# Performance work log

Hardware: AMD Instinct MI355X
Metric: run time of the kernel (lower is better)

Reference implementation:

```python
import jax, jax.numpy as jnp
import numpy as np

NODES_PER_GRAPH = 116
HEADS = 2
D_HEAD = 116  # out_channels per head
HID = 256
B = 512
N = B * NODES_PER_GRAPH
DEG = 8
E = N * DEG
D_OUT = HEADS * D_HEAD  # 232


def setup_inputs() -> dict:
    key = jax.random.key(0)
    ks = jax.random.split(key, 6)
    h_flat = jax.random.normal(ks[0], (N, HID), dtype=jnp.float32)
    # every node receives DEG edges from random nodes within its own 116-node graph
    dst = jnp.repeat(jnp.arange(N, dtype=jnp.int64), DEG)
    offs = jax.random.randint(ks[1], (E,), 0, NODES_PER_GRAPH, dtype=jnp.int64)
    src = (dst // NODES_PER_GRAPH) * NODES_PER_GRAPH + offs
    edge_index = jnp.stack([src, dst], axis=0)
    batch_index = jnp.repeat(jnp.arange(B, dtype=jnp.int64), NODES_PER_GRAPH)
    s = 1.0 / np.sqrt(HID)
    Wq = jax.random.normal(ks[2], (HID, D_OUT), dtype=jnp.float32) * s
    Wk = jax.random.normal(ks[3], (HID, D_OUT), dtype=jnp.float32) * s
    Wv = jax.random.normal(ks[4], (HID, D_OUT), dtype=jnp.float32) * s
    Ws = jax.random.normal(ks[5], (HID, D_OUT), dtype=jnp.float32) * s
    return {"h_flat": h_flat, "edge_index": edge_index, "batch_index": batch_index,
            "Wq": Wq, "Wk": Wk, "Wv": Wv, "Ws": Ws}


def _graph_transformer_layer(h, edge_index, Wq, Wk, Wv, Ws):
    # PyG TransformerConv-style multi-head edge attention, concat heads + root skip.
    n = h.shape[0]
    q = (h @ Wq).reshape(n, HEADS, D_HEAD)
    k = (h @ Wk).reshape(n, HEADS, D_HEAD)
    v = (h @ Wv).reshape(n, HEADS, D_HEAD)
    src, dst = edge_index[0], edge_index[1]
    # per-edge scores [E, H]
    scores = jnp.einsum('ehd,ehd->eh', q[dst], k[src]) / np.sqrt(D_HEAD)
    # segment softmax over incoming edges of each dst node
    m = jax.ops.segment_max(scores, dst, num_segments=n)
    m = jnp.where(jnp.isfinite(m), m, 0.0)
    ex = jnp.exp(scores - m[dst])
    denom = jax.ops.segment_sum(ex, dst, num_segments=n)
    alpha_e = ex / (denom[dst] + 1e-16)
    msg = alpha_e[:, :, None] * v[src]                      # [E, H, Dh]
    attn = jax.ops.segment_sum(msg, dst, num_segments=n)    # [N, H, Dh]
    return attn.reshape(n, D_OUT) + h @ Ws


def reference(h_flat, edge_index, batch_index, Wq, Wk, Wv, Ws):
    n = h_flat.shape[0]
    b = n // NODES_PER_GRAPH
    h_proj = _graph_transformer_layer(h_flat, edge_index, Wq, Wk, Wv, Ws)  # [N, 232]
    e = h_proj.mean(axis=-1)                                 # [N]
    # scatter_softmax over per-graph node segments
    em = jax.ops.segment_max(e, batch_index, num_segments=b)
    ee = jnp.exp(e - em[batch_index])
    es = jax.ops.segment_sum(ee, batch_index, num_segments=b)
    alpha = ee / es[batch_index]                             # [N]
    h_weighted = alpha[:, None] * h_proj                     # [N, 232]
    alpha_map = alpha.reshape(b, NODES_PER_GRAPH)            # [B, 116]
    return alpha_map, h_weighted
```

## Files before the change

### kernel.cpp

```cpp
#include <hip/hip_runtime.h>

#define NODES  116
#define HEADS  2
#define DH     116
#define HID    256
#define NGRAPH 512
#define NN     (NGRAPH*NODES)
#define DEG    8
#define DOUT   (HEADS*DH)
#define RSTR   136

typedef short  s8v  __attribute__((ext_vector_type(8)));
typedef float  f4v  __attribute__((ext_vector_type(4)));

static __device__ __forceinline__ float bf2f(unsigned short u) {
    union { unsigned int i; float f; } c; c.i = ((unsigned int)u) << 16; return c.f;
}
static __device__ __forceinline__ unsigned short f2bf(float f) {
    union { float f; unsigned int u; } c; c.f = f;
    unsigned int u = c.u;
    unsigned int r = (u + 0x7FFFu + ((u >> 16) & 1u)) >> 16;
    return (unsigned short)r;
}

#define GLD_LDS16(gptr, lptr) \
    __builtin_amdgcn_global_load_lds((const __attribute__((address_space(1))) void*)(gptr), \
                                     (__attribute__((address_space(3))) void*)(lptr), 16, 0, 0)

__global__ __launch_bounds__(256) void prep_w(const float* __restrict__ Wq,
                                              const float* __restrict__ Wk,
                                              const float* __restrict__ Wv,
                                              const float* __restrict__ Ws,
                                              unsigned short* __restrict__ wt)
{
    unsigned int f = blockIdx.x * 256 + threadIdx.x;
    unsigned int n    = f & 127;
    unsigned int quad = (f >> 7) & 3;
    unsigned int kb   = (f >> 9) & 7;
    unsigned int ch   = (f >> 12) & 3;
    unsigned int hd   = f >> 14;
    unsigned short o[8] = {0,0,0,0,0,0,0,0};
    if (n < NODES) {
        unsigned int col = hd * DH + n;
        unsigned int k   = kb * 32 + quad * 8;
        const float* W = (ch == 0) ? Wq : (ch == 1) ? Wk : (ch == 2) ? Wv : Ws;
        #pragma unroll
        for (int i = 0; i < 8; i++)
            o[i] = f2bf(W[(size_t)(k + i) * DOUT + col]);
    }
    *(uint4*)(wt + (size_t)f * 8) = *(const uint4*)o;
}

__global__ __launch_bounds__(1024, 4) void fused_all(
    const float* __restrict__ h,
    const unsigned short* __restrict__ wt,
    const int* __restrict__ eidx,
    unsigned short* __restrict__ hp,
    float* __restrict__ out_alpha,
    float* __restrict__ out_hw)
{
    __shared__ __align__(16) unsigned short stA[8*4096];
    __shared__ __align__(16) unsigned short ovl[2*128*RSTR];
    __shared__ int   srcl[NODES*DEG];
    __shared__ float scf[NODES*DEG];
    __shared__ float ps[2][NODES];
    __shared__ float red[2];

    unsigned short* const ql = ovl;
    unsigned short* const kl = ovl + 128 * RSTR;

    const int g   = blockIdx.x;
    const int tid = threadIdx.x;
    const int w    = tid >> 6;
    const int lane = tid & 63;
    const int l15  = lane & 15;
    const int quad = lane >> 4;
    const int wm   = w >> 2;
    const int wn   = w & 3;

    if (tid < NODES * DEG)
        srcl[tid] = eidx[(size_t)g * NODES * DEG + tid] - g * NODES;

    {
        const int am = tid >> 3;
        const int q8 = tid & 7;
        long grow = (long)g * NODES + am;
        if (grow >= NN) grow = NN - 1;
        const float* hrow = h + (size_t)grow * HID + q8 * 4;
        const int aoff = ((q8 >> 1) * 128 + am) * 8 + (q8 & 1) * 4;
        float4 a8[8];
        #pragma unroll
        for (int kb = 0; kb < 8; kb++) a8[kb] = *(const float4*)(hrow + kb * 32);
        #pragma unroll
        for (int kb = 0; kb < 8; kb++) {
            unsigned short o[4] = { f2bf(a8[kb].x), f2bf(a8[kb].y),
                                    f2bf(a8[kb].z), f2bf(a8[kb].w) };
            *(uint2*)(stA + kb * 4096 + aoff) = *(const uint2*)o;
        }
    }

    #pragma unroll
    for (int hd = 0; hd < 2; hd++) {
        const size_t wbase = (size_t)hd * 4 * 8 * 4096;

        f4v accq[2][2], acck[2][2], accv[2][2], accs[2][2];
        #pragma unroll
        for (int i = 0; i < 2; i++)
            #pragma unroll
            for (int j = 0; j < 2; j++)
                #pragma unroll
                for (int r = 0; r < 4; r++) {
                    accq[i][j][r] = 0.f; acck[i][j][r] = 0.f;
                    accv[i][j][r] = 0.f; accs[i][j][r] = 0.f;
                }

        #pragma unroll
        for (int j = 0; j < 2; j++) {
            int c = w * 2 + j;
            int ch = c >> 3, sub = c & 7;
            const unsigned short* src = wt + wbase + ((size_t)(ch * 8)) * 4096 + sub * 512;
            GLD_LDS16((const char*)src + lane * 16, (char*)ovl + c * 1024);
        }
        __syncthreads();

        #pragma unroll
        for (int kb = 0; kb < 8; kb++) {
            const unsigned short* curb = ovl + (kb & 1) * 16384;
            unsigned short* nxtb = ovl + ((kb & 1) ^ 1) * 16384;
            if (kb < 7) {
                #pragma unroll
                for (int j = 0; j < 2; j++) {
                    int c = w * 2 + j;
                    int ch = c >> 3, sub = c & 7;
                    const unsigned short* src = wt + wbase + ((size_t)(ch * 8 + kb + 1)) * 4096 + sub * 512;
                    GLD_LDS16((const char*)src + lane * 16, (char*)nxtb + c * 1024);
                }
            }
            const unsigned short* sa = stA + kb * 4096;
            s8v a0 = *(const s8v*)(sa + (quad * 128 + wm * 32 + l15) * 8);
            s8v a1 = *(const s8v*)(sa + (quad * 128 + wm * 32 + 16 + l15) * 8);
            #define CHUNK_MFMA(ACC, CH) { \
                s8v b0 = *(const s8v*)(curb + (CH) * 4096 + (quad * 128 + wn * 32 + l15) * 8); \
                s8v b1 = *(const s8v*)(curb + (CH) * 4096 + (quad * 128 + wn * 32 + 16 + l15) * 8); \
                ACC[0][0] = __builtin_amdgcn_mfma_f32_16x16x32_bf16(a0, b0, ACC[0][0], 0, 0, 0); \
                ACC[0][1] = __builtin_amdgcn_mfma_f32_16x16x32_bf16(a0, b1, ACC[0][1], 0, 0, 0); \
                ACC[1][0] = __builtin_amdgcn_mfma_f32_16x16x32_bf16(a1, b0, ACC[1][0], 0, 0, 0); \
                ACC[1][1] = __builtin_amdgcn_mfma_f32_16x16x32_bf16(a1, b1, ACC[1][1], 0, 0, 0); }
            CHUNK_MFMA(accq, 0)
            CHUNK_MFMA(acck, 1)
            CHUNK_MFMA(accv, 2)
            CHUNK_MFMA(accs, 3)
            #undef CHUNK_MFMA
            __syncthreads();
        }

        #pragma unroll
        for (int i = 0; i < 2; i++) {
            #pragma unroll
            for (int j = 0; j < 2; j++) {
                int col = wn * 32 + j * 16 + l15;
                #pragma unroll
                for (int r = 0; r < 4; r++) {
                    int row = wm * 32 + i * 16 + quad * 4 + r;
                    ql[row * RSTR + col] = (col < NODES) ? f2bf(accq[i][j][r]) : 0;
                    kl[row * RSTR + col] = (col < NODES) ? f2bf(acck[i][j][r]) : 0;
                }
            }
        }
        __syncthreads();

        f4v sacc[2][2];
        #pragma unroll
        for (int i = 0; i < 2; i++)
            #pragma unroll
            for (int j = 0; j < 2; j++)
                #pragma unroll
                for (int r = 0; r < 4; r++) sacc[i][j][r] = 0.f;
        #pragma unroll
        for (int ks = 0; ks < 4; ks++) {
            s8v a0 = *(const s8v*)(ql + (wm * 32 + l15) * RSTR + ks * 32 + quad * 8);
            s8v a1 = *(const s8v*)(ql + (wm * 32 + 16 + l15) * RSTR + ks * 32 + quad * 8);
            s8v b0 = *(const s8v*)(kl + (wn * 32 + l15) * RSTR + ks * 32 + quad * 8);
            s8v b1 = *(const s8v*)(kl + (wn * 32 + 16 + l15) * RSTR + ks * 32 + quad * 8);
            sacc[0][0] = __builtin_amdgcn_mfma_f32_16x16x32_bf16(a0, b0, sacc[0][0], 0, 0, 0);
            sacc[0][1] = __builtin_amdgcn_mfma_f32_16x16x32_bf16(a0, b1, sacc[0][1], 0, 0, 0);
            sacc[1][0] = __builtin_amdgcn_mfma_f32_16x16x32_bf16(a1, b0, sacc[1][0], 0, 0, 0);
            sacc[1][1] = __builtin_amdgcn_mfma_f32_16x16x32_bf16(a1, b1, sacc[1][1], 0, 0, 0);
        }
        #pragma unroll
        for (int i = 0; i < 2; i++) {
            #pragma unroll
            for (int r = 0; r < 4; r++) {
                int row = wm * 32 + i * 16 + quad * 4 + r;
                if (row < NODES) {
                    #pragma unroll
                    for (int j = 0; j < 2; j++) {
                        int col = wn * 32 + j * 16 + l15;
                        #pragma unroll
                        for (int e = 0; e < DEG; e++)
                            if (srcl[row * DEG + e] == col)
                                scf[row * DEG + e] = sacc[i][j][r];
                    }
                }
            }
        }
        __syncthreads();

        for (int f = tid; f < 128 * RSTR / 8; f += 1024)
            *(uint4*)(kl + (size_t)f * 8) = make_uint4(0u, 0u, 0u, 0u);
        #pragma unroll
        for (int i = 0; i < 2; i++) {
            #pragma unroll
            for (int j = 0; j < 2; j++) {
                int col = wn * 32 + j * 16 + l15;
                #pragma unroll
                for (int r = 0; r < 4; r++) {
                    int row = wm * 32 + i * 16 + quad * 4 + r;
                    ql[col * RSTR + row] = (row < NODES) ? f2bf(accv[i][j][r]) : 0;
                }
            }
        }
        __syncthreads();

        if (tid < NODES * DEG) {
            float s = scf[tid] * 0.09284766908852594f;
            float m = s;
            m = fmaxf(m, __shfl_xor(m, 1));
            m = fmaxf(m, __shfl_xor(m, 2));
            m = fmaxf(m, __shfl_xor(m, 4));
            float e = __expf(s - m);
            float sum = e;
            sum += __shfl_xor(sum, 1);
            sum += __shfl_xor(sum, 2);
            sum += __shfl_xor(sum, 4);
            scf[tid] = e / sum;
        }
        __syncthreads();

        if (tid < NODES) {
            #pragma unroll
            for (int j = 0; j < DEG; j++) {
                int sj = srcl[tid * DEG + j];
                bool first = true;
                for (int jj = 0; jj < j; jj++) first = first && (srcl[tid * DEG + jj] != sj);
                if (first) {
                    float a = scf[tid * DEG + j];
                    for (int jj = j + 1; jj < DEG; jj++)
                        if (srcl[tid * DEG + jj] == sj) a += scf[tid * DEG + jj];
                    kl[tid * RSTR + sj] = f2bf(a);
                }
            }
        }
        __syncthreads();

        #pragma unroll
        for (int ks = 0; ks < 4; ks++) {
            s8v a0 = *(const s8v*)(kl + (wm * 32 + l15) * RSTR + ks * 32 + quad * 8);
            s8v a1 = *(const s8v*)(kl + (wm * 32 + 16 + l15) * RSTR + ks * 32 + quad * 8);
            s8v b0 = *(const s8v*)(ql + (wn * 32 + l15) * RSTR + ks * 32 + quad * 8);
            s8v b1 = *(const s8v*)(ql + (wn * 32 + 16 + l15) * RSTR + ks * 32 + quad * 8);
            accs[0][0] = __builtin_amdgcn_mfma_f32_16x16x32_bf16(a0, b0, accs[0][0], 0, 0, 0);
            accs[0][1] = __builtin_amdgcn_mfma_f32_16x16x32_bf16(a0, b1, accs[0][1], 0, 0, 0);
            accs[1][0] = __builtin_amdgcn_mfma_f32_16x16x32_bf16(a1, b0, accs[1][0], 0, 0, 0);
            accs[1][1] = __builtin_amdgcn_mfma_f32_16x16x32_bf16(a1, b1, accs[1][1], 0, 0, 0);
        }
        __syncthreads();

        #pragma unroll
        for (int i = 0; i < 2; i++) {
            #pragma unroll
            for (int j = 0; j < 2; j++) {
                int col = wn * 32 + j * 16 + l15;
                #pragma unroll
                for (int r = 0; r < 4; r++) {
                    int row = wm * 32 + i * 16 + quad * 4 + r;
                    ql[row * RSTR + col] = f2bf(accs[i][j][r]);
                }
            }
        }
        __syncthreads();

        if (tid < NODES * DEG) {
            const int i   = tid >> 3;
            const int seg = tid & 7;
            float rs = 0.0f;
            #pragma unroll
            for (int t = 0; t < 2; t++) {
                int gi = seg + t * 8;
                if (gi < 15) {
                    const s8v v8 = *(const s8v*)(ql + i * RSTR + gi * 8);
                    #pragma unroll
                    for (int e = 0; e < 8; e++) rs += bf2f((unsigned short)v8[e]);
                }
            }
            rs += __shfl_xor(rs, 1);
            rs += __shfl_xor(rs, 2);
            rs += __shfl_xor(rs, 4);
            if (seg == 0) ps[hd][i] = rs;
        }
        if (hd == 0) {
            for (int f = tid; f < NODES * 29; f += 1024) {
                int r  = f / 29;
                int gi = f - r * 29;
                *(uint2*)(hp + ((size_t)g * NODES + r) * 116 + gi * 4) =
                    *(const uint2*)(ql + r * RSTR + gi * 4);
            }
        }
        __syncthreads();
    }

    if (tid < NODES) scf[tid] = (ps[0][tid] + ps[1][tid]) * (1.0f / DOUT);
    __syncthreads();
    if (tid < 64) {
        float a = scf[tid];
        float b = (tid + 64 < NODES) ? scf[tid + 64] : -1e30f;
        float mm = fmaxf(a, b);
        #pragma unroll
        for (int off = 32; off > 0; off >>= 1) mm = fmaxf(mm, __shfl_down(mm, off));
        if (tid == 0) red[0] = mm;
    }
    __syncthreads();
    if (tid < NODES) scf[tid] = __expf(scf[tid] - red[0]);
    __syncthreads();
    if (tid < 64) {
        float a = scf[tid] + ((tid + 64 < NODES) ? scf[tid + 64] : 0.0f);
        #pragma unroll
        for (int off = 32; off > 0; off >>= 1) a += __shfl_down(a, off);
        if (tid == 0) red[1] = a;
    }
    __syncthreads();
    if (tid < NODES) {
        float al = scf[tid] / red[1];
        scf[tid] = al;
        out_alpha[(size_t)g * NODES + tid] = al;
    }
    __syncthreads();
    for (int f = tid; f < NODES * 58; f += 1024) {
        int r  = f / 58;
        int gi = f - r * 58;
        float al = scf[r];
        float4 o;
        if (gi < 29) {
            uint2 hv = *(const uint2*)(hp + ((size_t)g * NODES + r) * 116 + gi * 4);
            o = make_float4(al * bf2f((unsigned short)(hv.x & 0xFFFF)),
                            al * bf2f((unsigned short)(hv.x >> 16)),
                            al * bf2f((unsigned short)(hv.y & 0xFFFF)),
                            al * bf2f((unsigned short)(hv.y >> 16)));
        } else {
            const unsigned short* hv = ql + r * RSTR + (gi - 29) * 4;
            o = make_float4(al * bf2f(hv[0]), al * bf2f(hv[1]),
                            al * bf2f(hv[2]), al * bf2f(hv[3]));
        }
        *(float4*)(out_hw + ((size_t)g * NODES + r) * DOUT + gi * 4) = o;
    }
}

extern "C" void kernel_launch(void* const* d_in, const int* in_sizes, int n_in,
                              void* d_out, int out_size, void* d_ws, size_t ws_size,
                              hipStream_t stream)
{
    const float* h    = (const float*)d_in[0];
    const int*   eidx = (const int*)d_in[1];
    const float* Wq   = (const float*)d_in[3];
    const float* Wk   = (const float*)d_in[4];
    const float* Wv   = (const float*)d_in[5];
    const float* Ws   = (const float*)d_in[6];

    unsigned short* wt = (unsigned short*)d_ws;
    unsigned short* hp = wt + (size_t)262144;

    float* out_alpha = (float*)d_out;
    float* out_hw    = out_alpha + NN;

    prep_w<<<128, 256, 0, stream>>>(Wq, Wk, Wv, Ws, wt);
    fused_all<<<NGRAPH, 1024, 0, stream>>>(h, wt, eidx, hp, out_alpha, out_hw);
}
```

Baseline: 219.2 us.

## Split fused graph kernel into GEMM, per-head attention, and pooling kernels

Replaces the single fused per-graph kernel with three kernels: a projection GEMM over (graph, head) blocks, a per-head attention kernel that writes projected rows and partial row sums, and a pooling kernel doing the per-graph softmax and weighted output. This doubles the block count so more work runs in parallel across CUs and lowers per-block shared memory. In exchange it adds global round trips for the QKVS and projected intermediates and extra launches. It falls back to the old fused kernel when the workspace is too small.

```diff
diff --git a/kernel.cpp b/kernel.cpp
--- a/kernel.cpp
+++ b/kernel.cpp
@@ -51,6 +51,343 @@
     *(uint4*)(wt + (size_t)f * 8) = *(const uint4*)o;
 }
 
+__global__ __launch_bounds__(1024, 8) void k1_gemm(
+    const float* __restrict__ h,
+    const unsigned short* __restrict__ wt,
+    unsigned short* __restrict__ qkvs)
+{
+    __shared__ __align__(16) unsigned short stA[8*4*116*8 + 96];
+    __shared__ __align__(16) unsigned short stB[2*4096];
+
+    const int b   = blockIdx.x;
+    const int g   = b >> 1;
+    const int hd  = b & 1;
+    const int tid = threadIdx.x;
+    const int w    = tid >> 6;
+    const int lane = tid & 63;
+    const int l15  = lane & 15;
+    const int quad = lane >> 4;
+    const int wm   = w >> 2;
+    const int wn   = w & 3;
+
+    {
+        const int am = tid >> 3;
+        const int q8 = tid & 7;
+        if (am < NODES) {
+            const float* hrow = h + ((size_t)g * NODES + am) * HID + q8 * 4;
+            #pragma unroll
+            for (int kb = 0; kb < 8; kb++) {
+                float4 av = *(const float4*)(hrow + kb * 32);
+                unsigned short o[4] = { f2bf(av.x), f2bf(av.y), f2bf(av.z), f2bf(av.w) };
+                *(uint2*)(stA + kb * (4*116*8) + ((q8 >> 1) * 116 + am) * 8 + (q8 & 1) * 4) =
+                    *(const uint2*)o;
+            }
+        }
+    }
+
+    const size_t wbase = (size_t)hd * 4 * 8 * 4096;
+
+    if (w < 8) {
+        const unsigned short* src = wt + wbase + w * 512;
+        GLD_LDS16((const char*)src + lane * 16, (char*)stB + w * 1024);
+    }
+    __syncthreads();
+
+    f4v acc[2][2];
+    #pragma unroll
+    for (int i = 0; i < 2; i++)
+        #pragma unroll
+        for (int j = 0; j < 2; j++)
+            #pragma unroll
+            for (int r = 0; r < 4; r++) acc[i][j][r] = 0.f;
+
+    for (int t = 0; t < 32; t++) {
+        const int kb = t & 7;
+        const unsigned short* cur = stB + (t & 1) * 4096;
+        if (t < 31 && w < 8) {
+            const unsigned short* src = wt + wbase + (size_t)(t + 1) * 4096 + w * 512;
+            GLD_LDS16((const char*)src + lane * 16,
+                      (char*)stB + ((t & 1) ^ 1) * 8192 + w * 1024);
+        }
+        const unsigned short* sa = stA + kb * (4*116*8);
+        s8v a0 = *(const s8v*)(sa + (quad * 116 + wm * 32 + l15) * 8);
+        s8v a1 = *(const s8v*)(sa + (quad * 116 + wm * 32 + 16 + l15) * 8);
+        s8v b0 = *(const s8v*)(cur + (quad * 128 + wn * 32 + l15) * 8);
+        s8v b1 = *(const s8v*)(cur + (quad * 128 + wn * 32 + 16 + l15) * 8);
+        acc[0][0] = __builtin_amdgcn_mfma_f32_16x16x32_bf16(a0, b0, acc[0][0], 0, 0, 0);
+        acc[0][1] = __builtin_amdgcn_mfma_f32_16x16x32_bf16(a0, b1, acc[0][1], 0, 0, 0);
+        acc[1][0] = __builtin_amdgcn_mfma_f32_16x16x32_bf16(a1, b0, acc[1][0], 0, 0, 0);
+        acc[1][1] = __builtin_amdgcn_mfma_f32_16x16x32_bf16(a1, b1, acc[1][1], 0, 0, 0);
+        if (kb == 7) {
+            const int ch = t >> 3;
+            #pragma unroll
+            for (int i = 0; i < 2; i++) {
+                #pragma unroll
+                for (int j = 0; j < 2; j++) {
+                    int col = wn * 32 + j * 16 + l15;
+                    #pragma unroll
+                    for (int r = 0; r < 4; r++) {
+                        int row = wm * 32 + i * 16 + quad * 4 + r;
+                        if (row < NODES && col < NODES)
+                            qkvs[(((size_t)g * NODES + row) * 2 + hd) * 464 + ch * 116 + col] =
+                                f2bf(acc[i][j][r]);
+                        acc[i][j][r] = 0.f;
+                    }
+                }
+            }
+        }
+        __syncthreads();
+    }
+}
+
+__global__ __launch_bounds__(1024, 8) void k2_attn(
+    const unsigned short* __restrict__ qkvs,
+    const int* __restrict__ eidx,
+    unsigned short* __restrict__ hpj,
+    float* __restrict__ psums)
+{
+    __shared__ __align__(16) unsigned short ql[128*RSTR];
+    __shared__ __align__(16) unsigned short kl[128*RSTR];
+    __shared__ int   srcl[NODES*DEG];
+    __shared__ float scf[NODES*DEG];
+
+    const int b   = blockIdx.x;
+    const int g   = b >> 1;
+    const int hd  = b & 1;
+    const int tid = threadIdx.x;
+    const int w    = tid >> 6;
+    const int lane = tid & 63;
+    const int l15  = lane & 15;
+    const int quad = lane >> 4;
+    const int wm   = w >> 2;
+    const int wn   = w & 3;
+
+    if (tid < NODES * DEG)
+        srcl[tid] = eidx[(size_t)g * NODES * DEG + tid] - g * NODES;
+
+    const size_t nb = ((size_t)g * NODES) * 2 + hd;
+
+    for (int f = tid; f < NODES * 29; f += 1024) {
+        int r = f / 29, c = f - r * 29;
+        *(uint2*)(ql + r * RSTR + c * 4) =
+            *(const uint2*)(qkvs + (nb + (size_t)r * 2) * 464 + 0 * 116 + c * 4);
+        *(uint2*)(kl + r * RSTR + c * 4) =
+            *(const uint2*)(qkvs + (nb + (size_t)r * 2) * 464 + 1 * 116 + c * 4);
+    }
+    for (int f = tid; f < 128 * 3; f += 1024) {
+        int r = f / 3, j = f - r * 3;
+        *(uint2*)(ql + r * RSTR + 116 + j * 4) = make_uint2(0u, 0u);
+        *(uint2*)(kl + r * RSTR + 116 + j * 4) = make_uint2(0u, 0u);
+    }
+    __syncthreads();
+
+    f4v sacc[2][2];
+    #pragma unroll
+    for (int i = 0; i < 2; i++)
+        #pragma unroll
+        for (int j = 0; j < 2; j++)
+            #pragma unroll
+            for (int r = 0; r < 4; r++) sacc[i][j][r] = 0.f;
+    #pragma unroll
+    for (int ks = 0; ks < 4; ks++) {
+        s8v a0 = *(const s8v*)(ql + (wm * 32 + l15) * RSTR + ks * 32 + quad * 8);
+        s8v a1 = *(const s8v*)(ql + (wm * 32 + 16 + l15) * RSTR + ks * 32 + quad * 8);
+        s8v b0 = *(const s8v*)(kl + (wn * 32 + l15) * RSTR + ks * 32 + quad * 8);
+        s8v b1 = *(const s8v*)(kl + (wn * 32 + 16 + l15) * RSTR + ks * 32 + quad * 8);
+        sacc[0][0] = __builtin_amdgcn_mfma_f32_16x16x32_bf16(a0, b0, sacc[0][0], 0, 0, 0);
+        sacc[0][1] = __builtin_amdgcn_mfma_f32_16x16x32_bf16(a0, b1, sacc[0][1], 0, 0, 0);
+        sacc[1][0] = __builtin_amdgcn_mfma_f32_16x16x32_bf16(a1, b0, sacc[1][0], 0, 0, 0);
+        sacc[1][1] = __builtin_amdgcn_mfma_f32_16x16x32_bf16(a1, b1, sacc[1][1], 0, 0, 0);
+    }
+    #pragma unroll
+    for (int i = 0; i < 2; i++) {
+        #pragma unroll
+        for (int r = 0; r < 4; r++) {
+            int row = wm * 32 + i * 16 + quad * 4 + r;
+            if (row < NODES) {
+                #pragma unroll
+                for (int j = 0; j < 2; j++) {
+                    int col = wn * 32 + j * 16 + l15;
+                    #pragma unroll
+                    for (int e = 0; e < DEG; e++)
+                        if (srcl[row * DEG + e] == col)
+                            scf[row * DEG + e] = sacc[i][j][r];
+                }
+            }
+        }
+    }
+    __syncthreads();
+
+    for (int f = tid; f < 128 * RSTR / 8; f += 1024)
+        *(uint4*)(kl + (size_t)f * 8) = make_uint4(0u, 0u, 0u, 0u);
+    for (int f = tid; f < NODES * 29; f += 1024) {
+        int r = f / 29, c = f - r * 29;
+        uint2 vv = *(const uint2*)(qkvs + (nb + (size_t)r * 2) * 464 + 2 * 116 + c * 4);
+        const unsigned short* vp = (const unsigned short*)&vv;
+        #pragma unroll
+        for (int i = 0; i < 4; i++)
+            ql[(c * 4 + i) * RSTR + r] = vp[i];
+    }
+    if (tid < 12 * 17) {
+        int r = 116 + tid / 17, c = tid - (tid / 17) * 17;
+        *(uint4*)(ql + r * RSTR + c * 8) = make_uint4(0u, 0u, 0u, 0u);
+    }
+    __syncthreads();
+
+    if (tid < NODES * DEG) {
+        float s = scf[tid] * 0.09284766908852594f;
+        float m = s;
+        m = fmaxf(m, __shfl_xor(m, 1));
+        m = fmaxf(m, __shfl_xor(m, 2));
+        m = fmaxf(m, __shfl_xor(m, 4));
+        float e = __expf(s - m);
+        float sum = e;
+        sum += __shfl_xor(sum, 1);
+        sum += __shfl_xor(sum, 2);
+        sum += __shfl_xor(sum, 4);
+        scf[tid] = e / sum;
+    }
+    __syncthreads();
+
+    if (tid < NODES) {
+        #pragma unroll
+        for (int j = 0; j < DEG; j++) {
+            int sj = srcl[tid * DEG + j];
+            bool first = true;
+            for (int jj = 0; jj < j; jj++) first = first && (srcl[tid * DEG + jj] != sj);
+            if (first) {
+                float a = scf[tid * DEG + j];
+                for (int jj = j + 1; jj < DEG; jj++)
+                    if (srcl[tid * DEG + jj] == sj) a += scf[tid * DEG + jj];
+                kl[tid * RSTR + sj] = f2bf(a);
+            }
+        }
+    }
+    __syncthreads();
+
+    f4v accs[2][2];
+    #pragma unroll
+    for (int i = 0; i < 2; i++)
+        #pragma unroll
+        for (int j = 0; j < 2; j++)
+            #pragma unroll
+            for (int r = 0; r < 4; r++) accs[i][j][r] = 0.f;
+    #pragma unroll
+    for (int ks = 0; ks < 4; ks++) {
+        s8v a0 = *(const s8v*)(kl + (wm * 32 + l15) * RSTR + ks * 32 + quad * 8);
+        s8v a1 = *(const s8v*)(kl + (wm * 32 + 16 + l15) * RSTR + ks * 32 + quad * 8);
+        s8v b0 = *(const s8v*)(ql + (wn * 32 + l15) * RSTR + ks * 32 + quad * 8);
+        s8v b1 = *(const s8v*)(ql + (wn * 32 + 16 + l15) * RSTR + ks * 32 + quad * 8);
+        accs[0][0] = __builtin_amdgcn_mfma_f32_16x16x32_bf16(a0, b0, accs[0][0], 0, 0, 0);
+        accs[0][1] = __builtin_amdgcn_mfma_f32_16x16x32_bf16(a0, b1, accs[0][1], 0, 0, 0);
+        accs[1][0] = __builtin_amdgcn_mfma_f32_16x16x32_bf16(a1, b0, accs[1][0], 0, 0, 0);
+        accs[1][1] = __builtin_amdgcn_mfma_f32_16x16x32_bf16(a1, b1, accs[1][1], 0, 0, 0);
+    }
+    __syncthreads();
+
+    for (int f = tid; f < NODES * 29; f += 1024) {
+        int r = f / 29, c = f - r * 29;
+        *(uint2*)(kl + r * RSTR + c * 4) =
+            *(const uint2*)(qkvs + (nb + (size_t)r * 2) * 464 + 3 * 116 + c * 4);
+    }
+    __syncthreads();
+
+    #pragma unroll
+    for (int i = 0; i < 2; i++) {
+        #pragma unroll
+        for (int j = 0; j < 2; j++) {
+            int col = wn * 32 + j * 16 + l15;
+            #pragma unroll
+            for (int r = 0; r < 4; r++) {
+                int row = wm * 32 + i * 16 + quad * 4 + r;
+                float v = accs[i][j][r];
+                if (row < NODES && col < NODES) v += bf2f(kl[row * RSTR + col]);
+                ql[row * RSTR + col] = f2bf(v);
+            }
+        }
+    }
+    __syncthreads();
+
+    if (tid < NODES * DEG) {
+        const int i   = tid >> 3;
+        const int seg = tid & 7;
+        float rs = 0.0f;
+        #pragma unroll
+        for (int t = 0; t < 2; t++) {
+            int gi = seg + t * 8;
+            if (gi < 15) {
+                const s8v v8 = *(const s8v*)(ql + i * RSTR + gi * 8);
+                #pragma unroll
+                for (int e = 0; e < 8; e++) rs += bf2f((unsigned short)v8[e]);
+            }
+        }
+        rs += __shfl_xor(rs, 1);
+        rs += __shfl_xor(rs, 2);
+        rs += __shfl_xor(rs, 4);
+        if (seg == 0) psums[((size_t)hd * NGRAPH + g) * NODES + i] = rs;
+    }
+    for (int f = tid; f < NODES * 29; f += 1024) {
+        int r  = f / 29;
+        int gi = f - r * 29;
+        *(uint2*)(hpj + ((size_t)(g * NODES + r)) * DOUT + hd * DH + gi * 4) =
+            *(const uint2*)(ql + r * RSTR + gi * 4);
+    }
+}
+
+__global__ __launch_bounds__(256) void pool_k3(const unsigned short* __restrict__ hp,
+                                               const float* __restrict__ psums,
+                                               float* __restrict__ out_alpha,
+                                               float* __restrict__ out_hw)
+{
+    __shared__ float ew[NODES];
+    __shared__ float alph[NODES];
+    __shared__ float red[2];
+
+    const int g   = blockIdx.x;
+    const int tid = threadIdx.x;
+
+    if (tid < NODES)
+        ew[tid] = (psums[(size_t)g * NODES + tid] +
+                   psums[((size_t)NGRAPH + g) * NODES + tid]) * (1.0f / DOUT);
+    __syncthreads();
+    if (tid < 64) {
+        float a = ew[tid];
+        float b = (tid + 64 < NODES) ? ew[tid + 64] : -1e30f;
+        float mm = fmaxf(a, b);
+        #pragma unroll
+        for (int off = 32; off > 0; off >>= 1) mm = fmaxf(mm, __shfl_down(mm, off));
+        if (tid == 0) red[0] = mm;
+    }
+    __syncthreads();
+    if (tid < NODES) ew[tid] = __expf(ew[tid] - red[0]);
+    __syncthreads();
+    if (tid < 64) {
+        float a = ew[tid] + ((tid + 64 < NODES) ? ew[tid + 64] : 0.0f);
+        #pragma unroll
+        for (int off = 32; off > 0; off >>= 1) a += __shfl_down(a, off);
+        if (tid == 0) red[1] = a;
+    }
+    __syncthreads();
+    if (tid < NODES) {
+        float al = ew[tid] / red[1];
+        alph[tid] = al;
+        out_alpha[(size_t)g * NODES + tid] = al;
+    }
+    __syncthreads();
+
+    for (int f = tid; f < NODES * 58; f += 256) {
+        int r  = f / 58;
+        int gi = f - r * 58;
+        float al = alph[r];
+        uint2 hv = *(const uint2*)(hp + ((size_t)(g * NODES + r)) * DOUT + gi * 4);
+        float4 o = make_float4(al * bf2f((unsigned short)(hv.x & 0xFFFF)),
+                               al * bf2f((unsigned short)(hv.x >> 16)),
+                               al * bf2f((unsigned short)(hv.y & 0xFFFF)),
+                               al * bf2f((unsigned short)(hv.y >> 16)));
+        *(float4*)(out_hw + ((size_t)(g * NODES + r)) * DOUT + gi * 4) = o;
+    }
+}
+
 __global__ __launch_bounds__(1024, 4) void fused_all(
     const float* __restrict__ h,
     const unsigned short* __restrict__ wt,
@@ -366,12 +703,26 @@
     const float* Wv   = (const float*)d_in[5];
     const float* Ws   = (const float*)d_in[6];
 
-    unsigned short* wt = (unsigned short*)d_ws;
-    unsigned short* hp = wt + (size_t)262144;
-
     float* out_alpha = (float*)d_out;
     float* out_hw    = out_alpha + NN;
 
+    const size_t WT_ELS   = 262144;
+    const size_t QKVS_ELS = (size_t)NN * 2 * 464;
+    const size_t HPJ_ELS  = (size_t)NN * DOUT;
+    const size_t NEED = (WT_ELS + QKVS_ELS + HPJ_ELS) * 2 + (size_t)2 * NGRAPH * NODES * 4;
+
+    unsigned short* wt = (unsigned short*)d_ws;
     prep_w<<<128, 256, 0, stream>>>(Wq, Wk, Wv, Ws, wt);
-    fused_all<<<NGRAPH, 1024, 0, stream>>>(h, wt, eidx, hp, out_alpha, out_hw);
+
+    if (ws_size >= NEED) {
+        unsigned short* qkvs = wt + WT_ELS;
+        unsigned short* hpj  = qkvs + QKVS_ELS;
+        float*          ps   = (float*)(hpj + HPJ_ELS);
+        k1_gemm<<<2*NGRAPH, 1024, 0, stream>>>(h, wt, qkvs);
+        k2_attn<<<2*NGRAPH, 1024, 0, stream>>>(qkvs, eidx, hpj, ps);
+        pool_k3<<<NGRAPH, 256, 0, stream>>>(hpj, ps, out_alpha, out_hw);
+    } else {
+        unsigned short* hp = wt + WT_ELS;
+        fused_all<<<NGRAPH, 1024, 0, stream>>>(h, wt, eidx, hp, out_alpha, out_hw);
+    }
 }
```

New measurement: 251.8 us. 1.15x slower.

## Split fused per-graph kernel into GEMM, edge-attention, and pooling kernels

Applied to the files above, without the earlier changes.

Replaces the single per-graph fused kernel with three kernels when the workspace is large enough. The first is a tiled bf16 MFMA GEMM writing Q/K/V/S to a global buffer. The second is a per-destination-node wavefront that computes edge scores, the softmax, aggregation and the skip add. The third does the per-graph pooling softmax and writes the outputs. This trades the fused kernel's poor occupancy and serialization for more parallel, better-tiled kernels, at the cost of extra global memory traffic (about 120 MB of bf16 intermediates) and additional launches.

```diff
diff --git a/kernel.cpp b/kernel.cpp
--- a/kernel.cpp
+++ b/kernel.cpp
@@ -51,6 +51,242 @@
     *(uint4*)(wt + (size_t)f * 8) = *(const uint4*)o;
 }
 
+__global__ __launch_bounds__(256, 4) void k_gemm(
+    const float* __restrict__ h,
+    const unsigned short* __restrict__ wt,
+    unsigned short* __restrict__ qkvs)
+{
+    __shared__ __align__(16) unsigned short lds[16384];
+    unsigned short* const A0 = lds;
+    unsigned short* const B0 = lds + 8192;
+
+    const int bid = blockIdx.x;
+    const int mt  = bid >> 3;
+    const int nt  = bid & 7;
+
+    const int tid  = threadIdx.x;
+    const int w    = tid >> 6;
+    const int lane = tid & 63;
+    const int l15  = lane & 15;
+    const int quad = lane >> 4;
+    const int wm2  = w >> 1;
+    const int wn2  = w & 1;
+
+    const int arow  = tid >> 1;
+    const int ahalf = tid & 1;
+    const float* hrow = h + ((size_t)mt * 128 + arow) * HID + ahalf * 16;
+    const int aq = ahalf * 2;
+    const unsigned short* wtb = wt + (size_t)nt * 8 * 4096;
+
+    f4v acc[4][4];
+    #pragma unroll
+    for (int i = 0; i < 4; i++)
+        #pragma unroll
+        for (int j = 0; j < 4; j++)
+            #pragma unroll
+            for (int r = 0; r < 4; r++) acc[i][j][r] = 0.f;
+
+    {
+        const char* src = (const char*)(wtb);
+        GLD_LDS16(src + tid * 16,         (char*)B0 + tid * 16);
+        GLD_LDS16(src + (tid + 256) * 16, (char*)B0 + (tid + 256) * 16);
+        float4 v0 = *(const float4*)(hrow + 0);
+        float4 v1 = *(const float4*)(hrow + 4);
+        float4 v2 = *(const float4*)(hrow + 8);
+        float4 v3 = *(const float4*)(hrow + 12);
+        unsigned short o[16] = { f2bf(v0.x),f2bf(v0.y),f2bf(v0.z),f2bf(v0.w),
+                                 f2bf(v1.x),f2bf(v1.y),f2bf(v1.z),f2bf(v1.w),
+                                 f2bf(v2.x),f2bf(v2.y),f2bf(v2.z),f2bf(v2.w),
+                                 f2bf(v3.x),f2bf(v3.y),f2bf(v3.z),f2bf(v3.w) };
+        *(uint4*)(A0 + ((aq    ) * 128 + arow) * 8) = *(const uint4*)(o);
+        *(uint4*)(A0 + ((aq + 1) * 128 + arow) * 8) = *(const uint4*)(o + 8);
+    }
+    __syncthreads();
+
+    #pragma unroll
+    for (int kb = 0; kb < 8; kb++) {
+        const int cur = kb & 1;
+        const int nxt = cur ^ 1;
+        float4 v0, v1, v2, v3;
+        if (kb < 7) {
+            const char* src = (const char*)(wtb + (size_t)(kb + 1) * 4096);
+            GLD_LDS16(src + tid * 16,         (char*)(B0 + nxt * 4096) + tid * 16);
+            GLD_LDS16(src + (tid + 256) * 16, (char*)(B0 + nxt * 4096) + (tid + 256) * 16);
+            v0 = *(const float4*)(hrow + (kb + 1) * 32);
+            v1 = *(const float4*)(hrow + (kb + 1) * 32 + 4);
+            v2 = *(const float4*)(hrow + (kb + 1) * 32 + 8);
+            v3 = *(const float4*)(hrow + (kb + 1) * 32 + 12);
+        }
+        const unsigned short* Ac = A0 + cur * 4096;
+        const unsigned short* Bc = B0 + cur * 4096;
+        s8v a0 = *(const s8v*)(Ac + (quad * 128 + wm2 * 64 +  0 + l15) * 8);
+        s8v a1 = *(const s8v*)(Ac + (quad * 128 + wm2 * 64 + 16 + l15) * 8);
+        s8v a2 = *(const s8v*)(Ac + (quad * 128 + wm2 * 64 + 32 + l15) * 8);
+        s8v a3 = *(const s8v*)(Ac + (quad * 128 + wm2 * 64 + 48 + l15) * 8);
+        #pragma unroll
+        for (int j = 0; j < 4; j++) {
+            s8v bj = *(const s8v*)(Bc + (quad * 128 + wn2 * 64 + j * 16 + l15) * 8);
+            acc[0][j] = __builtin_amdgcn_mfma_f32_16x16x32_bf16(a0, bj, acc[0][j], 0, 0, 0);
+            acc[1][j] = __builtin_amdgcn_mfma_f32_16x16x32_bf16(a1, bj, acc[1][j], 0, 0, 0);
+            acc[2][j] = __builtin_amdgcn_mfma_f32_16x16x32_bf16(a2, bj, acc[2][j], 0, 0, 0);
+            acc[3][j] = __builtin_amdgcn_mfma_f32_16x16x32_bf16(a3, bj, acc[3][j], 0, 0, 0);
+        }
+        if (kb < 7) {
+            unsigned short o[16] = { f2bf(v0.x),f2bf(v0.y),f2bf(v0.z),f2bf(v0.w),
+                                     f2bf(v1.x),f2bf(v1.y),f2bf(v1.z),f2bf(v1.w),
+                                     f2bf(v2.x),f2bf(v2.y),f2bf(v2.z),f2bf(v2.w),
+                                     f2bf(v3.x),f2bf(v3.y),f2bf(v3.z),f2bf(v3.w) };
+            *(uint4*)(A0 + nxt * 4096 + ((aq    ) * 128 + arow) * 8) = *(const uint4*)(o);
+            *(uint4*)(A0 + nxt * 4096 + ((aq + 1) * 128 + arow) * 8) = *(const uint4*)(o + 8);
+        }
+        __syncthreads();
+    }
+
+    unsigned short* cp = lds;
+    #pragma unroll
+    for (int i = 0; i < 4; i++)
+        #pragma unroll
+        for (int j = 0; j < 4; j++) {
+            int col = wn2 * 64 + j * 16 + l15;
+            #pragma unroll
+            for (int r = 0; r < 4; r++) {
+                int row = wm2 * 64 + i * 16 + quad * 4 + r;
+                cp[row * 128 + col] = f2bf(acc[i][j][r]);
+            }
+        }
+    __syncthreads();
+    const size_t outb = (size_t)mt * 128 * 1024 + (size_t)nt * 128;
+    #pragma unroll
+    for (int p = 0; p < 8; p++) {
+        int gi  = tid + p * 256;
+        int row = gi >> 4;
+        int cg  = gi & 15;
+        *(uint4*)(qkvs + outb + (size_t)row * 1024 + cg * 8) =
+            *(const uint4*)(cp + row * 128 + cg * 8);
+    }
+}
+
+__global__ __launch_bounds__(256) void k_score(
+    unsigned short* __restrict__ qkvs,
+    const int* __restrict__ eidx,
+    float* __restrict__ psums)
+{
+    const int wgid = blockIdx.x * 4 + (threadIdx.x >> 6);
+    const int dst  = wgid >> 1;
+    const int hd   = wgid & 1;
+    const int lane = threadIdx.x & 63;
+    const int grp  = lane >> 3;
+    const int sub  = lane & 7;
+    const int g    = dst / NODES;
+    const int node = dst - g * NODES;
+
+    const int src = eidx[(size_t)dst * DEG + grp];
+    const unsigned short* qr = qkvs + (size_t)dst * 1024 + hd * 512;
+    const unsigned short* kr = qkvs + (size_t)src * 1024 + hd * 512 + 128;
+
+    float d = 0.f;
+    #pragma unroll
+    for (int t = 0; t < 2; t++) {
+        s8v qv = *(const s8v*)(qr + sub * 8 + t * 64);
+        s8v kv = *(const s8v*)(kr + sub * 8 + t * 64);
+        #pragma unroll
+        for (int e = 0; e < 8; e++)
+            d += bf2f((unsigned short)qv[e]) * bf2f((unsigned short)kv[e]);
+    }
+    d += __shfl_xor(d, 1); d += __shfl_xor(d, 2); d += __shfl_xor(d, 4);
+
+    float s = d * 0.09284766908852594f;
+    float m = s;
+    m = fmaxf(m, __shfl_xor(m, 8));
+    m = fmaxf(m, __shfl_xor(m, 16));
+    m = fmaxf(m, __shfl_xor(m, 32));
+    float ex  = __expf(s - m);
+    float sum = ex;
+    sum += __shfl_xor(sum, 8); sum += __shfl_xor(sum, 16); sum += __shfl_xor(sum, 32);
+    float alpha = ex / sum;
+
+    const int d1ok = (lane + 64) < NODES;
+    float acc0 = 0.f, acc1 = 0.f;
+    #pragma unroll
+    for (int e = 0; e < 8; e++) {
+        float ae = __shfl(alpha, e * 8);
+        int   se = __shfl(src,   e * 8);
+        const unsigned short* vr = qkvs + (size_t)se * 1024 + hd * 512 + 256;
+        acc0 += ae * bf2f(vr[lane]);
+        if (d1ok) acc1 += ae * bf2f(vr[lane + 64]);
+    }
+    const size_t sbase = (size_t)dst * 1024 + hd * 512 + 384;
+    unsigned short b0 = f2bf(acc0 + bf2f(qkvs[sbase + lane]));
+    qkvs[sbase + lane] = b0;
+    float rs = bf2f(b0);
+    if (d1ok) {
+        unsigned short b1 = f2bf(acc1 + bf2f(qkvs[sbase + lane + 64]));
+        qkvs[sbase + lane + 64] = b1;
+        rs += bf2f(b1);
+    }
+    rs += __shfl_xor(rs, 1);  rs += __shfl_xor(rs, 2);  rs += __shfl_xor(rs, 4);
+    rs += __shfl_xor(rs, 8);  rs += __shfl_xor(rs, 16); rs += __shfl_xor(rs, 32);
+    if (lane == 0)
+        psums[((size_t)hd * NGRAPH + g) * NODES + node] = rs;
+}
+
+__global__ __launch_bounds__(256) void pool_k3(const unsigned short* __restrict__ qkvs,
+                                               const float* __restrict__ psums,
+                                               float* __restrict__ out_alpha,
+                                               float* __restrict__ out_hw)
+{
+    __shared__ float ew[NODES];
+    __shared__ float alph[NODES];
+    __shared__ float red[2];
+
+    const int g   = blockIdx.x;
+    const int tid = threadIdx.x;
+
+    if (tid < NODES)
+        ew[tid] = (psums[(size_t)g * NODES + tid] +
+                   psums[((size_t)NGRAPH + g) * NODES + tid]) * (1.0f / DOUT);
+    __syncthreads();
+    if (tid < 64) {
+        float a = ew[tid];
+        float b = (tid + 64 < NODES) ? ew[tid + 64] : -1e30f;
+        float mm = fmaxf(a, b);
+        #pragma unroll
+        for (int off = 32; off > 0; off >>= 1) mm = fmaxf(mm, __shfl_down(mm, off));
+        if (tid == 0) red[0] = mm;
+    }
+    __syncthreads();
+    if (tid < NODES) ew[tid] = __expf(ew[tid] - red[0]);
+    __syncthreads();
+    if (tid < 64) {
+        float a = ew[tid] + ((tid + 64 < NODES) ? ew[tid + 64] : 0.0f);
+        #pragma unroll
+        for (int off = 32; off > 0; off >>= 1) a += __shfl_down(a, off);
+        if (tid == 0) red[1] = a;
+    }
+    __syncthreads();
+    if (tid < NODES) {
+        float al = ew[tid] / red[1];
+        alph[tid] = al;
+        out_alpha[(size_t)g * NODES + tid] = al;
+    }
+    __syncthreads();
+
+    for (int f = tid; f < NODES * 58; f += 256) {
+        int r  = f / 58;
+        int gi = f - r * 58;
+        int d  = gi * 4;
+        float al = alph[r];
+        size_t row = ((size_t)g * NODES + r) * 1024;
+        size_t off = (d < DH) ? (size_t)(384 + d) : (size_t)(896 + d - DH);
+        uint2 hv = *(const uint2*)(qkvs + row + off);
+        float4 o = make_float4(al * bf2f((unsigned short)(hv.x & 0xFFFF)),
+                               al * bf2f((unsigned short)(hv.x >> 16)),
+                               al * bf2f((unsigned short)(hv.y & 0xFFFF)),
+                               al * bf2f((unsigned short)(hv.y >> 16)));
+        *(float4*)(out_hw + ((size_t)(g * NODES + r)) * DOUT + d) = o;
+    }
+}
+
 __global__ __launch_bounds__(1024, 4) void fused_all(
     const float* __restrict__ h,
     const unsigned short* __restrict__ wt,
@@ -366,12 +602,25 @@
     const float* Wv   = (const float*)d_in[5];
     const float* Ws   = (const float*)d_in[6];
 
-    unsigned short* wt = (unsigned short*)d_ws;
-    unsigned short* hp = wt + (size_t)262144;
-
     float* out_alpha = (float*)d_out;
     float* out_hw    = out_alpha + NN;
 
+    const size_t WT_ELS   = 262144;
+    const size_t QKVS_ELS = (size_t)NN * 1024;
+    const size_t PS_F32   = (size_t)2 * NGRAPH * NODES;
+    const size_t NEED = (WT_ELS + QKVS_ELS) * 2 + PS_F32 * 4;
+
+    unsigned short* wt = (unsigned short*)d_ws;
     prep_w<<<128, 256, 0, stream>>>(Wq, Wk, Wv, Ws, wt);
-    fused_all<<<NGRAPH, 1024, 0, stream>>>(h, wt, eidx, hp, out_alpha, out_hw);
-}
+
+    if (ws_size >= NEED) {
+        unsigned short* qkvs = wt + WT_ELS;
+        float*          ps   = (float*)(qkvs + QKVS_ELS);
+        k_gemm<<<464 * 8, 256, 0, stream>>>(h, wt, qkvs);
+        k_score<<<(NN * 2) / 4, 256, 0, stream>>>(qkvs, eidx, ps);
+        pool_k3<<<NGRAPH, 256, 0, stream>>>(qkvs, ps, out_alpha, out_hw);
+    } else {
+        unsigned short* hp = wt + WT_ELS;
+        fused_all<<<NGRAPH, 1024, 0, stream>>>(h, wt, eidx, hp, out_alpha, out_hw);
+    }
+}
```

Result: slower. 293.9 us (+34.1%).
